# Kernel optimization log

Measured on AMD Instinct MI355X. Metric: run time of the kernel, lower is better.

The kernel has to match this reference:

```python
import jax, jax.numpy as jnp
import numpy as np

B, N, F_IN = 8, 4096, 128
NT = B * N
E = 524288
H, C = 4, 64          # heads, per-head channels
D1 = H * C            # 256, conv1 out = conv2 in = conv2 out


def setup_inputs() -> dict:
    key = jax.random.key(0)
    ks = jax.random.split(key, 14)
    x = jax.random.normal(ks[0], (B, N, F_IN), dtype=jnp.float32)
    # within-graph random edges: E//B edges per graph, offset by graph id
    g = jnp.repeat(jnp.arange(B, dtype=jnp.int64), E // B)
    src = jax.random.randint(ks[1], (E,), 0, N, dtype=jnp.int64) + g * N
    dst = jax.random.randint(ks[2], (E,), 0, N, dtype=jnp.int64) + g * N
    edge_index = jnp.stack([src, dst])
    s = 0.05
    return {
        "x": x,
        "edge_index": edge_index,
        "W1": jax.random.normal(ks[3], (F_IN, D1)) * s,
        "att_src1": jax.random.normal(ks[4], (H, C)) * s,
        "att_dst1": jax.random.normal(ks[5], (H, C)) * s,
        "b1": jnp.zeros((D1,), jnp.float32),
        "W2": jax.random.normal(ks[6], (D1, D1)) * s,
        "att_src2": jax.random.normal(ks[7], (H, C)) * s,
        "att_dst2": jax.random.normal(ks[8], (H, C)) * s,
        "b2": jnp.zeros((D1,), jnp.float32),
        "pw1": jax.random.normal(ks[9], (D1, 1)) * s,
        "pb1": jnp.zeros((1,), jnp.float32),
        "pw2": jax.random.normal(ks[10], (D1, 1)) * s,
        "pb2": jnp.zeros((1,), jnp.float32),
    }


def _gat_conv(h, src, dst, W, att_src, att_dst, bias, n_nodes):
    """PyG GATConv (eval mode): linear, edge attention, segment softmax, scatter-add."""
    Hh, Cc = att_src.shape
    xp = (h @ W).reshape(n_nodes, Hh, Cc)              # [NT,H,C]
    a_src = jnp.sum(xp * att_src, axis=-1)             # [NT,H]
    a_dst = jnp.sum(xp * att_dst, axis=-1)             # [NT,H]
    logits = jax.nn.leaky_relu(a_src[src] + a_dst[dst], 0.2)   # [E',H]
    m = jax.lax.stop_gradient(jax.ops.segment_max(logits, dst, num_segments=n_nodes))
    e = jnp.exp(logits - m[dst])
    denom = jax.ops.segment_sum(e, dst, num_segments=n_nodes)
    alpha = e / (denom[dst] + 1e-16)                   # [E',H]
    msg = xp[src] * alpha[:, :, None]                  # [E',H,C]
    out = jax.ops.segment_sum(msg, dst, num_segments=n_nodes)
    return out.reshape(n_nodes, Hh * Cc) + bias


def reference(x, edge_index, W1, att_src1, att_dst1, b1, W2, att_src2, att_dst2, b2,
              pw1, pb1, pw2, pb2):
    b, n, f = x.shape
    nt = b * n
    xf = x.reshape(nt, f)
    loops = jnp.arange(nt, dtype=edge_index.dtype)     # add_self_loops=True (PyG default)
    src = jnp.concatenate([edge_index[0], loops])
    dst = jnp.concatenate([edge_index[1], loops])

    x0 = jnp.mean(x, axis=-1)                          # [B,N]
    h1 = jax.nn.elu(_gat_conv(xf, src, dst, W1, att_src1, att_dst1, b1, nt))
    x1 = (h1 @ pw1 + pb1)[:, 0].reshape(b, n)          # pool1
    h2 = jax.nn.elu(_gat_conv(h1, src, dst, W2, att_src2, att_dst2, b2, nt))
    x2 = (h2 @ pw2 + pb2)[:, 0].reshape(b, n)          # pool2
    # with_layer_norm==True (bool) != 'True' (str) -> layer norm skipped, which_layer='all'
    return jnp.concatenate([x0, x1, x2], axis=1)       # [B, 3N]
```

## Files before the change

kernel.cpp:

```cpp
#include <hip/hip_runtime.h>

typedef __attribute__((ext_vector_type(8))) short bf16x8;
typedef __attribute__((ext_vector_type(4))) float f32x4;
typedef __attribute__((ext_vector_type(2))) float pk2;

constexpr int B    = 8;
constexpr int N    = 4096;
constexpr int FIN  = 128;
constexpr int NT   = B * N;
constexpr int H    = 4;
constexpr int C    = 64;
constexpr int D1   = H * C;
constexpr int E    = 524288;
constexpr int ETOT = E + NT;
constexpr int NSLOT = 18;
constexpr int CAP  = 64;

__device__ __forceinline__ unsigned short f2bf(float f) {
    unsigned u = __float_as_uint(f);
    return (unsigned short)((u + 0x7FFFu + ((u >> 16) & 1u)) >> 16);
}
__device__ __forceinline__ float bf2f(unsigned short b) {
    return __uint_as_float(((unsigned)b) << 16);
}

__global__ __launch_bounds__(256) void k_zero(unsigned* __restrict__ cnt,
                                              float* __restrict__ asrc,
                                              unsigned short* __restrict__ xpb) {
    int g = blockIdx.x & 7, j = blockIdx.x >> 3;
    int i = (g << 12) + (j << 8) + threadIdx.x;
    cnt[i] = 0u;
    if (i < 4)  asrc[NT * H + i] = -1e30f;
    if (i < 64) reinterpret_cast<uint2*>(xpb)[(size_t)NT * 64 + i] = make_uint2(0u, 0u);
}

__device__ __forceinline__ void pack_body(
    const float* __restrict__ W, const float* __restrict__ as_,
    const float* __restrict__ ad_, unsigned short* __restrict__ pB, int g)
{
    int kt  = g / (NSLOT * 64);
    int rem = g % (NSLOT * 64);
    int slot = rem >> 6, l = rem & 63;
    int k0 = kt * 32 + 8 * (l >> 4);
    bool wantLo = (slot == 17);
    int nt = wantLo ? 16 : slot;
    int n  = nt * 16 + (l & 15);
    bf16x8 o;
    #pragma unroll
    for (int j = 0; j < 8; ++j) {
        int k = k0 + j;
        float v;
        if (n < 256) {
            v = W[k * D1 + n];
        } else if (n < 264) {
            int idx = n - 256, hh = idx & 3;
            const float* av = (idx < 4) ? as_ : ad_;
            float s = 0.f;
            #pragma unroll 8
            for (int c = 0; c < C; ++c) s += W[k * D1 + hh * C + c] * av[hh * C + c];
            v = s;
        } else {
            v = 0.f;
        }
        unsigned short hb = f2bf(v);
        o[j] = wantLo ? (short)f2bf(v - bf2f(hb)) : (short)hb;
    }
    *reinterpret_cast<bf16x8*>(pB + (size_t)g * 8) = o;
}

__global__ __launch_bounds__(256) void k_combo(
    const float* __restrict__ x, const int* __restrict__ ei,
    unsigned short* __restrict__ hi, unsigned short* __restrict__ lo,
    float* __restrict__ out, unsigned* __restrict__ cnt, int* __restrict__ slots,
    const float* __restrict__ W1, const float* __restrict__ as1, const float* __restrict__ ad1,
    const float* __restrict__ W2, const float* __restrict__ as2, const float* __restrict__ ad2,
    unsigned short* __restrict__ pB1, unsigned short* __restrict__ pB2)
{
    int bid = blockIdx.x, t = threadIdx.x;

    if (bid < 54) {
        if (bid < 18) pack_body(W1, as1, ad1, pB1, bid * 256 + t);
        else          pack_body(W2, as2, ad2, pB2, (bid - 18) * 256 + t);
        return;
    }

    int nb = bid - 54;
    int g  = nb & 7, loc = nb >> 3;

    {
        int node = (g << 12) + (loc << 3) + (t >> 5);
        int q = t & 31;
        float4 v = reinterpret_cast<const float4*>(x)[node * 32 + q];
        ushort4 h, l;
        h.x = f2bf(v.x); l.x = f2bf(v.x - bf2f(h.x));
        h.y = f2bf(v.y); l.y = f2bf(v.y - bf2f(h.y));
        h.z = f2bf(v.z); l.z = f2bf(v.z - bf2f(h.z));
        h.w = f2bf(v.w); l.w = f2bf(v.w - bf2f(h.w));
        reinterpret_cast<ushort4*>(hi)[node * 32 + q] = h;
        reinterpret_cast<ushort4*>(lo)[node * 32 + q] = l;
        float s = v.x + v.y + v.z + v.w;
        #pragma unroll
        for (int o = 16; o; o >>= 1) s += __shfl_xor(s, o);
        if (q == 0) {
            int n = node & (N - 1);
            out[g * (3 * N) + n] = s * (1.0f / 128.0f);
        }
    }

    if (nb < 2176) {
        int eb;
        if (nb < 2048) eb = (g << 8) + (nb >> 3);
        else           eb = 2048 + (g << 4) + ((nb - 2048) >> 3);
        int e = eb * 256 + t;
        int s, d;
        if (e < E) { s = ei[e]; d = ei[E + e]; } else { s = d = e - E; }
        unsigned p = atomicAdd(cnt + d, 1u);
        slots[d * CAP + p] = s * 4;
    }
}

template <int K, bool PAD>
__global__ __launch_bounds__(256) void k_mfma(
    const unsigned short* __restrict__ Ahi, const unsigned short* __restrict__ Alo,
    const unsigned short* __restrict__ pB,
    unsigned short* __restrict__ xpb, float* __restrict__ asrc, float* __restrict__ adst,
    const unsigned* __restrict__ cnt, int* __restrict__ slots)
{
    constexpr int KT = K / 32;
    int t = threadIdx.x, lane = t & 63, w = t >> 6;

    if (PAD && blockIdx.x >= NT / 64) {
        int bl = blockIdx.x - NT / 64;
        int node = ((bl & 7) << 12) + ((bl >> 3) << 8) + t;
        int deg = (int)cnt[node];
        int dpad = ((deg + 1) & ~1) + 14;
        int* sl = slots + (size_t)node * CAP;
        for (int i = deg; i < dpad; ++i) sl[i] = NT * 4;
        return;
    }

    int wm = w & 1, wn = w >> 1;
    int m0 = ((blockIdx.x & 7) << 12) + ((blockIdx.x >> 3) << 6) + wm * 32;
    int sBase = wn * 9;

    f32x4 acc[2][9];
    #pragma unroll
    for (int i = 0; i < 2; ++i)
        #pragma unroll
        for (int j = 0; j < 9; ++j)
            acc[i][j] = (f32x4){0.f, 0.f, 0.f, 0.f};

    int aRow = m0 + (lane & 15);
    int aCol = 8 * (lane >> 4);
    const unsigned short* a0h = Ahi + (size_t)aRow * K + aCol;
    const unsigned short* a0l = Alo + (size_t)aRow * K + aCol;
    const unsigned short* bp  = pB + ((size_t)sBase * 64 + lane) * 8;

    bf16x8 bc[9], bn[9];
    bf16x8 ah0c, al0c, ah1c, al1c, ah0n, al0n, ah1n, al1n;

    #pragma unroll
    for (int j = 0; j < 9; ++j) bc[j] = *reinterpret_cast<const bf16x8*>(bp + j * 512);
    ah0c = *reinterpret_cast<const bf16x8*>(a0h);
    al0c = *reinterpret_cast<const bf16x8*>(a0l);
    ah1c = *reinterpret_cast<const bf16x8*>(a0h + 16 * K);
    al1c = *reinterpret_cast<const bf16x8*>(a0l + 16 * K);

    #pragma unroll
    for (int kt = 0; kt < KT; ++kt) {
        if (kt + 1 < KT) {
            const unsigned short* bpn = bp + (size_t)(kt + 1) * NSLOT * 64 * 8;
            #pragma unroll
            for (int j = 0; j < 9; ++j) bn[j] = *reinterpret_cast<const bf16x8*>(bpn + j * 512);
            ah0n = *reinterpret_cast<const bf16x8*>(a0h + (kt + 1) * 32);
            al0n = *reinterpret_cast<const bf16x8*>(a0l + (kt + 1) * 32);
            ah1n = *reinterpret_cast<const bf16x8*>(a0h + 16 * K + (kt + 1) * 32);
            al1n = *reinterpret_cast<const bf16x8*>(a0l + 16 * K + (kt + 1) * 32);
        }
        __builtin_amdgcn_sched_barrier(0);
        if (wn == 0) {
            #pragma unroll
            for (int j = 0; j < 9; ++j) {
                acc[0][j] = __builtin_amdgcn_mfma_f32_16x16x32_bf16(ah0c, bc[j], acc[0][j], 0, 0, 0);
                acc[1][j] = __builtin_amdgcn_mfma_f32_16x16x32_bf16(ah1c, bc[j], acc[1][j], 0, 0, 0);
                acc[0][j] = __builtin_amdgcn_mfma_f32_16x16x32_bf16(al0c, bc[j], acc[0][j], 0, 0, 0);
                acc[1][j] = __builtin_amdgcn_mfma_f32_16x16x32_bf16(al1c, bc[j], acc[1][j], 0, 0, 0);
            }
        } else {
            #pragma unroll
            for (int j = 0; j < 8; ++j) {
                acc[0][j] = __builtin_amdgcn_mfma_f32_16x16x32_bf16(ah0c, bc[j], acc[0][j], 0, 0, 0);
                acc[1][j] = __builtin_amdgcn_mfma_f32_16x16x32_bf16(ah1c, bc[j], acc[1][j], 0, 0, 0);
                acc[0][j] = __builtin_amdgcn_mfma_f32_16x16x32_bf16(al0c, bc[j], acc[0][j], 0, 0, 0);
                acc[1][j] = __builtin_amdgcn_mfma_f32_16x16x32_bf16(al1c, bc[j], acc[1][j], 0, 0, 0);
            }
            acc[0][7] = __builtin_amdgcn_mfma_f32_16x16x32_bf16(ah0c, bc[8], acc[0][7], 0, 0, 0);
            acc[1][7] = __builtin_amdgcn_mfma_f32_16x16x32_bf16(ah1c, bc[8], acc[1][7], 0, 0, 0);
        }
        if (kt + 1 < KT) {
            #pragma unroll
            for (int j = 0; j < 9; ++j) bc[j] = bn[j];
            ah0c = ah0n; al0c = al0n; ah1c = ah1n; al1c = al1n;
        }
    }

    #pragma unroll
    for (int mt = 0; mt < 2; ++mt) {
        int rowB = m0 + mt * 16 + (lane >> 4) * 4;
        if (wn == 0) {
            #pragma unroll
            for (int j = 0; j < 9; ++j) {
                int col = j * 16 + (lane & 15);
                #pragma unroll
                for (int r = 0; r < 4; ++r)
                    xpb[(size_t)(rowB + r) * D1 + col] = f2bf(acc[mt][j][r]);
            }
        } else {
            #pragma unroll
            for (int j = 0; j < 8; ++j) {
                int nt = 9 + j;
                int col = nt * 16 + (lane & 15);
                #pragma unroll
                for (int r = 0; r < 4; ++r) {
                    int row = rowB + r;
                    float v = acc[mt][j][r];
                    if (col < 256)      xpb[(size_t)row * D1 + col] = f2bf(v);
                    else if (col < 260) asrc[row * H + (col - 256)] = v;
                    else if (col < 264) adst[row * H + (col - 260)] = v;
                }
            }
        }
    }
}

__global__ __launch_bounds__(256) void k_node(
    const unsigned* __restrict__ cnt, const int* __restrict__ slots,
    const float* __restrict__ asrc, const float* __restrict__ adst,
    const unsigned short* __restrict__ xp,
    const float* __restrict__ bias, const float* __restrict__ pw,
    const float* __restrict__ pb,
    unsigned short* __restrict__ hhi, unsigned short* __restrict__ hlo,
    float* __restrict__ out, int sec)
{
    int bid = blockIdx.x;
    int w = threadIdx.x >> 6, lane = threadIdx.x & 63;
    int half = lane >> 5;
    int hl   = lane & 31;
    int head = hl >> 3;
    int node = ((bid & 7) << 12) | (((bid >> 3) << 2) + w);

    int deg = (int)cnt[node];
    int dp  = (deg + 1) & ~1;
    const int* sl = slots + (size_t)node * CAP;
    float adh = adst[node * H + head];
    const uint4* xp4 = (const uint4*)xp;

    float den = 0.f;
    pk2 acc01 = {0.f, 0.f}, acc23 = {0.f, 0.f}, acc45 = {0.f, 0.f}, acc67 = {0.f, 0.f};

    #define PROC(aa, vv)                                                     \
    {                                                                        \
        float l  = aa + adh;                                                 \
        float ev = __expf(fmaxf(l, 0.2f * l));                               \
        den += ev;                                                           \
        pk2 e2 = {ev, ev};                                                   \
        pk2 t01 = {__uint_as_float(vv.x << 16), __uint_as_float(vv.x & 0xFFFF0000u)}; \
        pk2 t23 = {__uint_as_float(vv.y << 16), __uint_as_float(vv.y & 0xFFFF0000u)}; \
        pk2 t45 = {__uint_as_float(vv.z << 16), __uint_as_float(vv.z & 0xFFFF0000u)}; \
        pk2 t67 = {__uint_as_float(vv.w << 16), __uint_as_float(vv.w & 0xFFFF0000u)}; \
        acc01 = __builtin_elementwise_fma(e2, t01, acc01);                   \
        acc23 = __builtin_elementwise_fma(e2, t23, acc23);                   \
        acc45 = __builtin_elementwise_fma(e2, t45, acc45);                   \
        acc67 = __builtin_elementwise_fma(e2, t67, acc67);                   \
    }

    int   s_;
    float aX, aY, aZ, a_;
    uint4 vX, vY, vZ, v_;
    s_ = sl[0 + half]; aX = asrc[s_ + head]; vX = xp4[(s_ << 3) + hl];
    s_ = sl[2 + half]; aY = asrc[s_ + head]; vY = xp4[(s_ << 3) + hl];
    s_ = sl[4 + half]; aZ = asrc[s_ + head]; vZ = xp4[(s_ << 3) + hl];

    for (int i = 0; i < dp; i += 6) {
        s_ = sl[i + 6 + half];  a_ = asrc[s_ + head]; v_ = xp4[(s_ << 3) + hl];
        PROC(aX, vX); aX = a_; vX = v_;
        s_ = sl[i + 8 + half];  a_ = asrc[s_ + head]; v_ = xp4[(s_ << 3) + hl];
        PROC(aY, vY); aY = a_; vY = v_;
        s_ = sl[i + 10 + half]; a_ = asrc[s_ + head]; v_ = xp4[(s_ << 3) + hl];
        PROC(aZ, vZ); aZ = a_; vZ = v_;
    }
    #undef PROC

    den      += __shfl_xor(den, 32);
    acc01[0] += __shfl_xor(acc01[0], 32);
    acc01[1] += __shfl_xor(acc01[1], 32);
    acc23[0] += __shfl_xor(acc23[0], 32);
    acc23[1] += __shfl_xor(acc23[1], 32);
    acc45[0] += __shfl_xor(acc45[0], 32);
    acc45[1] += __shfl_xor(acc45[1], 32);
    acc67[0] += __shfl_xor(acc67[0], 32);
    acc67[1] += __shfl_xor(acc67[1], 32);

    float invd = 1.f / (den + 1e-16f);
    float4 b0 = reinterpret_cast<const float4*>(bias)[hl * 2];
    float4 b1 = reinterpret_cast<const float4*>(bias)[hl * 2 + 1];
    float4 p0 = reinterpret_cast<const float4*>(pw)[hl * 2];
    float4 p1 = reinterpret_cast<const float4*>(pw)[hl * 2 + 1];

    float h0 = fmaf(acc01[0], invd, b0.x), h1 = fmaf(acc01[1], invd, b0.y),
          h2 = fmaf(acc23[0], invd, b0.z), h3 = fmaf(acc23[1], invd, b0.w),
          h4 = fmaf(acc45[0], invd, b1.x), h5 = fmaf(acc45[1], invd, b1.y),
          h6 = fmaf(acc67[0], invd, b1.z), h7 = fmaf(acc67[1], invd, b1.w);
    h0 = h0 > 0.f ? h0 : __expf(h0) - 1.f;
    h1 = h1 > 0.f ? h1 : __expf(h1) - 1.f;
    h2 = h2 > 0.f ? h2 : __expf(h2) - 1.f;
    h3 = h3 > 0.f ? h3 : __expf(h3) - 1.f;
    h4 = h4 > 0.f ? h4 : __expf(h4) - 1.f;
    h5 = h5 > 0.f ? h5 : __expf(h5) - 1.f;
    h6 = h6 > 0.f ? h6 : __expf(h6) - 1.f;
    h7 = h7 > 0.f ? h7 : __expf(h7) - 1.f;

    if (hhi && half == 0) {
        unsigned short q0 = f2bf(h0), q1 = f2bf(h1), q2 = f2bf(h2), q3 = f2bf(h3),
                       q4 = f2bf(h4), q5 = f2bf(h5), q6 = f2bf(h6), q7 = f2bf(h7);
        uint4 hw, lw;
        hw.x = (unsigned)q0 | ((unsigned)q1 << 16);
        hw.y = (unsigned)q2 | ((unsigned)q3 << 16);
        hw.z = (unsigned)q4 | ((unsigned)q5 << 16);
        hw.w = (unsigned)q6 | ((unsigned)q7 << 16);
        lw.x = (unsigned)f2bf(h0 - bf2f(q0)) | ((unsigned)f2bf(h1 - bf2f(q1)) << 16);
        lw.y = (unsigned)f2bf(h2 - bf2f(q2)) | ((unsigned)f2bf(h3 - bf2f(q3)) << 16);
        lw.z = (unsigned)f2bf(h4 - bf2f(q4)) | ((unsigned)f2bf(h5 - bf2f(q5)) << 16);
        lw.w = (unsigned)f2bf(h6 - bf2f(q6)) | ((unsigned)f2bf(h7 - bf2f(q7)) << 16);
        reinterpret_cast<uint4*>(hhi)[node * 32 + hl] = hw;
        reinterpret_cast<uint4*>(hlo)[node * 32 + hl] = lw;
    }

    float p = h0 * p0.x + h1 * p0.y + h2 * p0.z + h3 * p0.w
            + h4 * p1.x + h5 * p1.y + h6 * p1.z + h7 * p1.w;
    #pragma unroll
    for (int o = 16; o; o >>= 1) p += __shfl_xor(p, o);
    if (lane == 0) {
        int b = node >> 12;
        int n = node & (N - 1);
        out[b * (3 * N) + sec * N + n] = p + pb[0];
    }
}

extern "C" void kernel_launch(void* const* d_in, const int* in_sizes, int n_in,
                              void* d_out, int out_size, void* d_ws, size_t ws_size,
                              hipStream_t stream) {
    const float* x   = (const float*)d_in[0];
    const int*   ei  = (const int*)d_in[1];
    const float* W1  = (const float*)d_in[2];
    const float* as1 = (const float*)d_in[3];
    const float* ad1 = (const float*)d_in[4];
    const float* b1  = (const float*)d_in[5];
    const float* W2  = (const float*)d_in[6];
    const float* as2 = (const float*)d_in[7];
    const float* ad2 = (const float*)d_in[8];
    const float* b2  = (const float*)d_in[9];
    const float* pw1 = (const float*)d_in[10];
    const float* pb1 = (const float*)d_in[11];
    const float* pw2 = (const float*)d_in[12];
    const float* pb2 = (const float*)d_in[13];
    float* out = (float*)d_out;

    unsigned short* xpb  = (unsigned short*)d_ws;
    unsigned short* xhi  = xpb  + (size_t)(NT + 1) * D1;
    unsigned short* xlo  = xhi  + (size_t)NT * FIN;
    unsigned short* h1hi = xlo  + (size_t)NT * FIN;
    unsigned short* h1lo = h1hi + (size_t)NT * D1;
    float*    asrc   = (float*)(h1lo + (size_t)NT * D1);
    float*    adst   = asrc + (size_t)(NT + 1) * H;
    unsigned short* pB1 = (unsigned short*)(adst + (size_t)NT * H);
    unsigned short* pB2 = pB1 + (size_t)4 * NSLOT * 64 * 8;
    unsigned* cnt    = (unsigned*)(pB2 + (size_t)8 * NSLOT * 64 * 8);
    int*      slots  = (int*)(cnt + NT);

    k_zero<<<NT / 256, 256, 0, stream>>>(cnt, asrc, xpb);
    k_combo<<<54 + NT / 8, 256, 0, stream>>>(x, ei, xhi, xlo, out, cnt, slots,
                                             W1, as1, ad1, W2, as2, ad2, pB1, pB2);

    k_mfma<128, true><<<NT / 64 + NT / 256, 256, 0, stream>>>(
        xhi, xlo, pB1, xpb, asrc, adst, cnt, slots);
    k_node<<<NT / 4, 256, 0, stream>>>(cnt, slots, asrc, adst, xpb,
                                       b1, pw1, pb1, h1hi, h1lo, out, 1);

    k_mfma<256, false><<<NT / 64, 256, 0, stream>>>(
        h1hi, h1lo, pB2, xpb, asrc, adst, cnt, slots);
    k_node<<<NT / 4, 256, 0, stream>>>(cnt, slots, asrc, adst, xpb,
                                       b2, pw2, pb2, nullptr, nullptr, out, 2);
}
```

Baseline: 133.7 us.

## Bucket edges per graph with LDS atomics and drop the zeroing kernel

```diff
diff --git a/kernel.cpp b/kernel.cpp
--- a/kernel.cpp
+++ b/kernel.cpp
@@ -12,7 +12,7 @@
 constexpr int C    = 64;
 constexpr int D1   = H * C;
 constexpr int E    = 524288;
-constexpr int ETOT = E + NT;
+constexpr int EPB  = E / B;
 constexpr int NSLOT = 18;
 constexpr int CAP  = 64;
 
@@ -22,16 +22,6 @@
 }
 __device__ __forceinline__ float bf2f(unsigned short b) {
     return __uint_as_float(((unsigned)b) << 16);
-}
-
-__global__ __launch_bounds__(256) void k_zero(unsigned* __restrict__ cnt,
-                                              float* __restrict__ asrc,
-                                              unsigned short* __restrict__ xpb) {
-    int g = blockIdx.x & 7, j = blockIdx.x >> 3;
-    int i = (g << 12) + (j << 8) + threadIdx.x;
-    cnt[i] = 0u;
-    if (i < 4)  asrc[NT * H + i] = -1e30f;
-    if (i < 64) reinterpret_cast<uint2*>(xpb)[(size_t)NT * 64 + i] = make_uint2(0u, 0u);
 }
 
 __device__ __forceinline__ void pack_body(
@@ -74,48 +64,71 @@
     float* __restrict__ out, unsigned* __restrict__ cnt, int* __restrict__ slots,
     const float* __restrict__ W1, const float* __restrict__ as1, const float* __restrict__ ad1,
     const float* __restrict__ W2, const float* __restrict__ as2, const float* __restrict__ ad2,
-    unsigned short* __restrict__ pB1, unsigned short* __restrict__ pB2)
+    unsigned short* __restrict__ pB1, unsigned short* __restrict__ pB2,
+    float* __restrict__ asrc, unsigned short* __restrict__ xpb)
 {
+    __shared__ unsigned lcnt[N];
     int bid = blockIdx.x, t = threadIdx.x;
 
-    if (bid < 54) {
-        if (bid < 18) pack_body(W1, as1, ad1, pB1, bid * 256 + t);
-        else          pack_body(W2, as2, ad2, pB2, (bid - 18) * 256 + t);
+    if (bid < 8) {
+        int g = bid;
+        for (int i = t; i < N; i += 256) {
+            lcnt[i] = 1u;
+            int node = (g << 12) + i;
+            slots[(size_t)node * CAP] = node * 4;
+        }
+        __syncthreads();
+        const int* srcp = ei + (size_t)g * EPB;
+        const int* dstp = ei + E + (size_t)g * EPB;
+        for (int base = 0; base < EPB; base += 1024) {
+            int i0 = base + t;
+            int s0 = srcp[i0], d0 = dstp[i0];
+            int s1 = srcp[i0 + 256], d1 = dstp[i0 + 256];
+            int s2 = srcp[i0 + 512], d2 = dstp[i0 + 512];
+            int s3 = srcp[i0 + 768], d3 = dstp[i0 + 768];
+            unsigned p0 = atomicAdd(&lcnt[d0 & (N - 1)], 1u);
+            unsigned p1 = atomicAdd(&lcnt[d1 & (N - 1)], 1u);
+            unsigned p2 = atomicAdd(&lcnt[d2 & (N - 1)], 1u);
+            unsigned p3 = atomicAdd(&lcnt[d3 & (N - 1)], 1u);
+            slots[(size_t)d0 * CAP + p0] = s0 * 4;
+            slots[(size_t)d1 * CAP + p1] = s1 * 4;
+            slots[(size_t)d2 * CAP + p2] = s2 * 4;
+            slots[(size_t)d3 * CAP + p3] = s3 * 4;
+        }
+        __syncthreads();
+        for (int i = t; i < N; i += 256) cnt[(g << 12) + i] = lcnt[i];
         return;
     }
 
-    int nb = bid - 54;
+    if (bid < 62) {
+        int pb = bid - 8;
+        if (pb == 0) {
+            if (t < 4)  asrc[NT * H + t] = -1e30f;
+            if (t < 64) reinterpret_cast<uint2*>(xpb)[(size_t)NT * 64 + t] = make_uint2(0u, 0u);
+        }
+        if (pb < 18) pack_body(W1, as1, ad1, pB1, pb * 256 + t);
+        else         pack_body(W2, as2, ad2, pB2, (pb - 18) * 256 + t);
+        return;
+    }
+
+    int nb = bid - 62;
     int g  = nb & 7, loc = nb >> 3;
-
-    {
-        int node = (g << 12) + (loc << 3) + (t >> 5);
-        int q = t & 31;
-        float4 v = reinterpret_cast<const float4*>(x)[node * 32 + q];
-        ushort4 h, l;
-        h.x = f2bf(v.x); l.x = f2bf(v.x - bf2f(h.x));
-        h.y = f2bf(v.y); l.y = f2bf(v.y - bf2f(h.y));
-        h.z = f2bf(v.z); l.z = f2bf(v.z - bf2f(h.z));
-        h.w = f2bf(v.w); l.w = f2bf(v.w - bf2f(h.w));
-        reinterpret_cast<ushort4*>(hi)[node * 32 + q] = h;
-        reinterpret_cast<ushort4*>(lo)[node * 32 + q] = l;
-        float s = v.x + v.y + v.z + v.w;
-        #pragma unroll
-        for (int o = 16; o; o >>= 1) s += __shfl_xor(s, o);
-        if (q == 0) {
-            int n = node & (N - 1);
-            out[g * (3 * N) + n] = s * (1.0f / 128.0f);
-        }
-    }
-
-    if (nb < 2176) {
-        int eb;
-        if (nb < 2048) eb = (g << 8) + (nb >> 3);
-        else           eb = 2048 + (g << 4) + ((nb - 2048) >> 3);
-        int e = eb * 256 + t;
-        int s, d;
-        if (e < E) { s = ei[e]; d = ei[E + e]; } else { s = d = e - E; }
-        unsigned p = atomicAdd(cnt + d, 1u);
-        slots[d * CAP + p] = s * 4;
+    int node = (g << 12) + (loc << 3) + (t >> 5);
+    int q = t & 31;
+    float4 v = reinterpret_cast<const float4*>(x)[node * 32 + q];
+    ushort4 h, l;
+    h.x = f2bf(v.x); l.x = f2bf(v.x - bf2f(h.x));
+    h.y = f2bf(v.y); l.y = f2bf(v.y - bf2f(h.y));
+    h.z = f2bf(v.z); l.z = f2bf(v.z - bf2f(h.z));
+    h.w = f2bf(v.w); l.w = f2bf(v.w - bf2f(h.w));
+    reinterpret_cast<ushort4*>(hi)[node * 32 + q] = h;
+    reinterpret_cast<ushort4*>(lo)[node * 32 + q] = l;
+    float s = v.x + v.y + v.z + v.w;
+    #pragma unroll
+    for (int o = 16; o; o >>= 1) s += __shfl_xor(s, o);
+    if (q == 0) {
+        int n = node & (N - 1);
+        out[g * (3 * N) + n] = s * (1.0f / 128.0f);
     }
 }
 
@@ -378,9 +391,9 @@
     unsigned* cnt    = (unsigned*)(pB2 + (size_t)8 * NSLOT * 64 * 8);
     int*      slots  = (int*)(cnt + NT);
 
-    k_zero<<<NT / 256, 256, 0, stream>>>(cnt, asrc, xpb);
-    k_combo<<<54 + NT / 8, 256, 0, stream>>>(x, ei, xhi, xlo, out, cnt, slots,
-                                             W1, as1, ad1, W2, as2, ad2, pB1, pB2);
+    k_combo<<<62 + NT / 8, 256, 0, stream>>>(x, ei, xhi, xlo, out, cnt, slots,
+                                             W1, as1, ad1, W2, as2, ad2, pB1, pB2,
+                                             asrc, xpb);
 
     k_mfma<128, true><<<NT / 64 + NT / 256, 256, 0, stream>>>(
         xhi, xlo, pB1, xpb, asrc, adst, cnt, slots);
```

Result: slower. 147.3 us (+10.1%).
